# Kernel optimization log

Hardware: AMD Instinct MI355X
Metric: run time of the kernel (lower is better)

The kernel has to match this reference:

```python
import jax, jax.numpy as jnp
import numpy as np

N, E, B = 50000, 800000, 64
F_IN, HID, H, L = 128, 128, 4, 4
C = HID // H  # per-head channels = 32
NEG_SLOPE = 0.2  # PyG GATConv default leaky_relu slope


def setup_inputs() -> dict:
    key = jax.random.key(0)
    ks = iter(jax.random.split(key, 32))
    rn = lambda shape, s=0.05: jax.random.normal(next(ks), shape, jnp.float32) * s
    x = jax.random.normal(next(ks), (N, F_IN), jnp.float32)
    edge_index = jax.random.randint(next(ks), (2, E), 0, N, jnp.int32)
    edge_attr = jax.random.uniform(next(ks), (E, 2), dtype=jnp.float32)
    batch = jnp.sort(jax.random.randint(next(ks), (N,), 0, B, jnp.int32))
    return {
        "x": x, "edge_attr": edge_attr,
        "Win": rn((F_IN, HID)), "b_in": jnp.zeros((HID,), jnp.float32),
        "We1": rn((2, 16)), "be1": jnp.zeros((16,), jnp.float32),
        "We2": rn((16, H)), "be2": jnp.zeros((H,), jnp.float32),
        "Wl": rn((L, HID, HID)), "a_src": rn((L, H, C)), "a_dst": rn((L, H, C)),
        "bl": jnp.zeros((L, HID), jnp.float32),
        "ln_g": jnp.ones((L, HID), jnp.float32), "ln_b": jnp.zeros((L, HID), jnp.float32),
        "Wg1": rn((HID, HID // 2)), "bg1": jnp.zeros((HID // 2,), jnp.float32),
        "Wg2": rn((HID // 2, 1)), "bg2": jnp.zeros((1,), jnp.float32),
        "edge_index": edge_index, "batch": batch,
    }


def _layer_norm(x, g, b, eps=1e-5):
    mu = x.mean(-1, keepdims=True)
    var = ((x - mu) ** 2).mean(-1, keepdims=True)
    return (x - mu) * jax.lax.rsqrt(var + eps) * g + b


def _gat_conv(h, src, dst, W, a_s, a_d, bias):
    # PyG GATConv (shared lin for src/dst), add_self_loops already in src/dst.
    xp = (h @ W).reshape(N, H, C)            # [N,H,C]
    as_n = (xp * a_s).sum(-1)                # [N,H]
    ad_n = (xp * a_d).sum(-1)                # [N,H]
    e = jax.nn.leaky_relu(as_n[src] + ad_n[dst], NEG_SLOPE)   # [E+N,H]
    m = jax.ops.segment_max(e, dst, num_segments=N)           # stable softmax per dst
    p = jnp.exp(e - m[dst])
    s = jax.ops.segment_sum(p, dst, num_segments=N)
    alpha = p / (s[dst] + 1e-16)
    out = jax.ops.segment_sum(xp[src] * alpha[..., None], dst, num_segments=N)
    return out.reshape(N, HID) + bias


def reference(x, edge_attr, Win, b_in, We1, be1, We2, be2, Wl, a_src, a_dst, bl,
              ln_g, ln_b, Wg1, bg1, Wg2, bg2, edge_index, batch):
    h = x @ Win + b_in                                   # input_proj
    # edge bias MLP -> per-edge scalar -> scatter_add crit_signal (no self loops)
    edge_bias = jax.nn.relu(edge_attr @ We1 + be1) @ We2 + be2   # [E,H]
    edge_scalar = edge_bias.mean(axis=1)                         # [E]
    crit = jnp.zeros((N,), h.dtype).at[edge_index[1]].add(edge_scalar)[:, None]
    # self loops for GATConv
    loop = jnp.arange(N, dtype=edge_index.dtype)
    src = jnp.concatenate([edge_index[0], loop])
    dst = jnp.concatenate([edge_index[1], loop])
    for i in range(L):  # fixed small layer count
        h_new = _gat_conv(h, src, dst, Wl[i], a_src[i], a_dst[i], bl[i])
        h_new = _layer_norm(h_new, ln_g[i], ln_b[i])
        h_new = h_new + crit                             # broadcast [N,1]
        h = h_new + h                                    # residual (shapes match); dropout=eval noop
    # GlobalAttention pooling: softmax(gate) over each graph, weighted sum
    gate = jnp.tanh(h @ Wg1 + bg1) @ Wg2 + bg2           # [N,1]
    gmax = jax.ops.segment_max(gate, batch, num_segments=B)
    gp = jnp.exp(gate - gmax[batch])
    gs = jax.ops.segment_sum(gp, batch, num_segments=B)
    gate_sm = gp / (gs[batch] + 1e-16)
    return jax.ops.segment_sum(gate_sm * h, batch, num_segments=B)   # [B,HID]
```

## Files before the change

### kernel.cpp

```cpp
#include <hip/hip_runtime.h>
#include <math.h>

#define N_NODES 50000
#define N_EDGES 800000
#define N_B     64

typedef __attribute__((ext_vector_type(8))) short v8s;
typedef __attribute__((ext_vector_type(4))) float v4f;

__device__ __forceinline__ float lrelu(float x){ return x > 0.f ? x : 0.2f*x; }
__device__ __forceinline__ unsigned short f2b(float f){
  unsigned u = __float_as_uint(f);
  return (unsigned short)((u + 0x7fffu + ((u >> 16) & 1u)) >> 16);
}
__device__ __forceinline__ float blo(unsigned u){ return __uint_as_float(u << 16); }
__device__ __forceinline__ float bhi(unsigned u){ return __uint_as_float(u & 0xffff0000u); }

__global__ void k_conv(const float* __restrict__ Win, const float* __restrict__ Wl,
                       const float* __restrict__ a_src, const float* __restrict__ a_dst,
                       const float* __restrict__ Wg1,
                       unsigned short* __restrict__ WinT, unsigned short* __restrict__ WlT,
                       unsigned short* __restrict__ Wg1T){
  int i = blockIdx.x*256 + threadIdx.x;
  if (i < 16384){
    int n = i >> 7, k = i & 127;
    WinT[n*128+k] = f2b(Win[k*128+n]);
    return;
  }
  i -= 16384;
  if (i < 65536){
    int l = i >> 14, n = (i >> 7) & 127, k = i & 127;
    WlT[l*144*128 + n*128 + k] = f2b(Wl[l*16384 + k*128 + n]);
    return;
  }
  i -= 65536;
  if (i < 4096){
    int l = i >> 10, k = (i >> 3) & 127, t = i & 7;
    int hh = t & 3, sd = t >> 2;
    const float* av = (sd ? a_dst : a_src) + l*128 + hh*32;
    const float* wr = Wl + l*16384 + k*128 + hh*32;
    float s = 0.f;
    #pragma unroll
    for (int c = 0; c < 32; c++) s = fmaf(wr[c], av[c], s);
    WlT[l*144*128 + (128 + sd*4 + hh)*128 + k] = f2b(s);
    return;
  }
  i -= 4096;
  if (i < 4096){
    int l = i >> 10, r = (i >> 7) & 7, k = i & 127;
    WlT[l*144*128 + (136+r)*128 + k] = 0;
    return;
  }
  i -= 4096;
  if (i < 8192){
    int n = i >> 7, k = i & 127;
    Wg1T[n*128+k] = f2b(Wg1[k*64+n]);
  }
}

__global__ void k_setup(const int* __restrict__ batch, int* __restrict__ start,
                        int* __restrict__ cnt){
  int i = blockIdx.x*256 + threadIdx.x;
  if (i >= N_NODES) return;
  cnt[i] = 0;
  int b = batch[i];
  int bp = (i == 0) ? -1 : batch[i-1];
  for (int j = bp+1; j <= b; j++) start[j] = i;
  if (i == N_NODES-1){
    for (int j = b+1; j <= N_B; j++) start[j] = N_NODES;
  }
}

__global__ void k_hist(const int* __restrict__ ei, int* __restrict__ cnt, int* __restrict__ rank){
  int t = blockIdx.x*256 + threadIdx.x;
  if (t >= 200000) return;
  #pragma unroll
  for (int r = 0; r < 4; r++){
    int e = t + r*200000;
    int d = ei[N_EDGES + e];
    rank[e] = atomicAdd(&cnt[d], 1);
  }
}

__global__ void k_scan1(const int* __restrict__ cnt, int* __restrict__ incl, int* __restrict__ part){
  __shared__ int sh[256];
  int tid = threadIdx.x, i = blockIdx.x*256 + tid;
  int v = (i < N_NODES) ? cnt[i] : 0;
  sh[tid] = v; __syncthreads();
  for (int off = 1; off < 256; off <<= 1){
    int t = (tid >= off) ? sh[tid-off] : 0;
    __syncthreads();
    sh[tid] += t; __syncthreads();
  }
  if (i < N_NODES) incl[i] = sh[tid];
  if (tid == 255) part[blockIdx.x] = sh[255];
}
__global__ void k_scan23(const int* __restrict__ cnt, const int* __restrict__ incl,
                         const int* __restrict__ part, int* __restrict__ off){
  __shared__ int red[4];
  __shared__ int bsum;
  int tid = threadIdx.x, lane = tid & 63, wave = tid >> 6;
  int v = (tid < (int)blockIdx.x) ? part[tid] : 0;
  #pragma unroll
  for (int m = 1; m < 64; m <<= 1) v += __shfl_xor(v, m);
  if (lane == 0) red[wave] = v;
  __syncthreads();
  if (tid == 0) bsum = red[0]+red[1]+red[2]+red[3];
  __syncthreads();
  int i = blockIdx.x*256 + tid;
  if (i >= N_NODES) return;
  int e = incl[i] - cnt[i] + bsum;
  off[i] = e;
  if (i == N_NODES-1) off[N_NODES] = e + cnt[i];
}

__global__ void k_fill(const float* __restrict__ ea, const float* __restrict__ We1,
                       const float* __restrict__ be1, const float* __restrict__ We2,
                       const float* __restrict__ be2, const int* __restrict__ ei,
                       const int* __restrict__ off, const int* __restrict__ rank,
                       int2* __restrict__ es){
  __shared__ float w0[16], w1[16], bb[16], w2s[16];
  __shared__ float b2s;
  int tid = threadIdx.x;
  if (tid < 16){
    w0[tid] = We1[tid]; w1[tid] = We1[16+tid]; bb[tid] = be1[tid];
    w2s[tid] = 0.25f*(We2[tid*4]+We2[tid*4+1]+We2[tid*4+2]+We2[tid*4+3]);
  }
  if (tid == 0) b2s = 0.25f*(be2[0]+be2[1]+be2[2]+be2[3]);
  __syncthreads();
  int t = blockIdx.x*256 + tid;
  if (t >= 200000) return;
  #pragma unroll
  for (int r = 0; r < 4; r++){
    int e = t + r*200000;
    float a0 = ea[2*e], a1 = ea[2*e+1];
    float s = b2s;
    #pragma unroll
    for (int j = 0; j < 16; j++){
      float v = fmaf(a0, w0[j], fmaf(a1, w1[j], bb[j]));
      v = v > 0.f ? v : 0.f;
      s = fmaf(v, w2s[j], s);
    }
    int d = ei[N_EDGES + e];
    int p = off[d] + rank[e];
    es[p] = make_int2(ei[e], __float_as_int(s));
  }
}

template<int NT, int MODE, bool AF32>
__global__ __launch_bounds__(256) void k_mgemm(
    const void* __restrict__ A, const unsigned short* __restrict__ Bt,
    const float* __restrict__ bias,
    float* __restrict__ h, unsigned short* __restrict__ hb,
    unsigned short* __restrict__ xpb, float* __restrict__ asn, float* __restrict__ adn,
    const float* __restrict__ Wg2, const float* __restrict__ bg2, float* __restrict__ gate)
{
  __shared__ __attribute__((aligned(16))) unsigned short Bs[NT*16][136];
  __shared__ __attribute__((aligned(16))) unsigned short As[4][16][136];
  int tid = threadIdx.x, wave = tid >> 6, lane = tid & 63;
  int l15 = lane & 15, quad = lane >> 4;
  int rbase = blockIdx.x * 64;
  for (int id = tid; id < NT*16*16; id += 256){
    int r = id >> 4, ch = id & 15;
    *(v8s*)&Bs[r][ch*8] = *(const v8s*)(Bt + r*128 + ch*8);
  }
  for (int id = tid; id < 64*16; id += 256){
    int r = id >> 4, ch = id & 15;
    int gr = rbase + r;
    v8s v = {0,0,0,0,0,0,0,0};
    if (gr < N_NODES){
      if (AF32){
        const float* Af = (const float*)A + (size_t)gr*128 + ch*8;
        float4 va = *(const float4*)Af;
        float4 vb = *(const float4*)(Af + 4);
        v[0]=(short)f2b(va.x); v[1]=(short)f2b(va.y); v[2]=(short)f2b(va.z); v[3]=(short)f2b(va.w);
        v[4]=(short)f2b(vb.x); v[5]=(short)f2b(vb.y); v[6]=(short)f2b(vb.z); v[7]=(short)f2b(vb.w);
      } else {
        v = *(const v8s*)((const unsigned short*)A + (size_t)gr*128 + ch*8);
      }
    }
    *(v8s*)&As[r >> 4][r & 15][ch*8] = v;
  }
  __syncthreads();
  v4f acc[NT];
  #pragma unroll
  for (int t = 0; t < NT; t++) acc[t] = (v4f){0.f,0.f,0.f,0.f};
  #pragma unroll
  for (int kb = 0; kb < 4; kb++){
    v8s a = *(v8s*)&As[wave][l15][kb*32 + quad*8];
    #pragma unroll
    for (int ct = 0; ct < NT; ct++){
      v8s b = *(v8s*)&Bs[ct*16 + l15][kb*32 + quad*8];
      acc[ct] = __builtin_amdgcn_mfma_f32_16x16x32_bf16(a, b, acc[ct], 0, 0, 0);
    }
  }
  int row0 = rbase + wave*16 + quad*4;
  if (MODE == 0){
    #pragma unroll
    for (int ct = 0; ct < 8; ct++){
      float bcol = bias[ct*16 + l15];
      #pragma unroll
      for (int r = 0; r < 4; r++){
        int gr = row0 + r;
        if (gr < N_NODES){
          float v = acc[ct][r] + bcol;
          h[(size_t)gr*128 + ct*16 + l15] = v;
          hb[(size_t)gr*128 + ct*16 + l15] = f2b(v);
        }
      }
    }
  } else if (MODE == 1){
    #pragma unroll
    for (int ct = 0; ct < 8; ct++){
      #pragma unroll
      for (int r = 0; r < 4; r++){
        int gr = row0 + r;
        if (gr < N_NODES) xpb[(size_t)gr*128 + ct*16 + l15] = f2b(acc[ct][r]);
      }
    }
    #pragma unroll
    for (int r = 0; r < 4; r++){
      int gr = row0 + r;
      if (gr < N_NODES){
        float v = acc[NT-1][r];
        if (l15 < 4) asn[gr*4 + l15] = v;
        else if (l15 < 8) adn[gr*4 + (l15-4)] = v;
      }
    }
  } else {
    float part[4] = {0.f,0.f,0.f,0.f};
    #pragma unroll
    for (int ct = 0; ct < NT; ct++){
      float b1 = bias[ct*16 + l15];
      float w2 = Wg2[ct*16 + l15];
      #pragma unroll
      for (int r = 0; r < 4; r++) part[r] = fmaf(tanhf(acc[ct][r] + b1), w2, part[r]);
    }
    #pragma unroll
    for (int m = 1; m < 16; m <<= 1){
      #pragma unroll
      for (int r = 0; r < 4; r++) part[r] += __shfl_xor(part[r], m);
    }
    if (l15 == 0){
      float b2 = bg2[0];
      #pragma unroll
      for (int r = 0; r < 4; r++){
        int gr = row0 + r;
        if (gr < N_NODES) gate[gr] = part[r] + b2;
      }
    }
  }
}

template<bool CRIT>
__global__ __launch_bounds__(256) void k_aggr(
    const unsigned short* __restrict__ xpb, const float* __restrict__ asn,
    const float* __restrict__ adn, const int* __restrict__ off,
    const int2* __restrict__ es,
    const float* __restrict__ bl, const float* __restrict__ lng,
    const float* __restrict__ lnb, float* __restrict__ crit,
    float* __restrict__ h, unsigned short* __restrict__ hb)
{
  __shared__ float lp[4][256];
  int wave = threadIdx.x >> 6, lane = threadIdx.x & 63;
  int n = blockIdx.x*4 + wave;
  if (n >= N_NODES) return;
  int base = off[n], deg = off[n+1] - base;
  float4 ad4 = *(const float4*)(adn + n*4);
  float4 asf = *(const float4*)(asn + n*4);
  float ex = lrelu(asf.x+ad4.x), ey = lrelu(asf.y+ad4.y);
  float ez = lrelu(asf.z+ad4.z), ew = lrelu(asf.w+ad4.w);
  const unsigned* xw = (const unsigned*)xpb;
  float* myp = &lp[wave][0];
  int hh = lane >> 4;
  float acc0, acc1, sx, sy, sz, sw, cr;
  float psx, psy, psz, psw;

  if (deg <= 64){
    int sreg = 0;
    float e0 = -3.0e38f, e1 = -3.0e38f, e2 = -3.0e38f, e3 = -3.0e38f;
    float cw = 0.f;
    if (lane < deg){
      int2 er = es[base + lane];
      sreg = er.x;
      float4 a = *(const float4*)(asn + sreg*4);
      e0 = lrelu(a.x+ad4.x); e1 = lrelu(a.y+ad4.y);
      e2 = lrelu(a.z+ad4.z); e3 = lrelu(a.w+ad4.w);
      if (CRIT) cw = __int_as_float(er.y);
    }
    float mx = fmaxf(e0,ex), my = fmaxf(e1,ey), mz = fmaxf(e2,ez), mw = fmaxf(e3,ew);
    #pragma unroll
    for (int m = 1; m < 64; m <<= 1){
      mx = fmaxf(mx, __shfl_xor(mx, m)); my = fmaxf(my, __shfl_xor(my, m));
      mz = fmaxf(mz, __shfl_xor(mz, m)); mw = fmaxf(mw, __shfl_xor(mw, m));
      if (CRIT) cw += __shfl_xor(cw, m);
    }
    if (CRIT){ if (lane == 0) crit[n] = cw; cr = cw; }
    else cr = crit[n];
    psx = __expf(ex-mx); psy = __expf(ey-my); psz = __expf(ez-mz); psw = __expf(ew-mw);
    float p0 = 0.f, p1 = 0.f, p2 = 0.f, p3 = 0.f;
    if (lane < deg){
      p0 = __expf(e0-mx); p1 = __expf(e1-my); p2 = __expf(e2-mz); p3 = __expf(e3-mw);
    }
    sx = p0; sy = p1; sz = p2; sw = p3;
    *(float4*)(&myp[4*lane]) = make_float4(p0,p1,p2,p3);
    __threadfence_block();
    float pself = hh < 2 ? (hh == 0 ? psx : psy) : (hh == 2 ? psz : psw);
    unsigned us = (xw + ((size_t)(unsigned)n << 6))[lane];
    acc0 = pself * blo(us); acc1 = pself * bhi(us);
    int degR = (deg + 7) & ~7;
    for (int c = 0; c < degR; c += 8){
      unsigned u[8];
      #pragma unroll
      for (int k = 0; k < 8; k++){
        int s0 = __builtin_amdgcn_readlane(sreg, c + k);
        u[k] = (xw + ((size_t)(unsigned)s0 << 6))[lane];
      }
      #pragma unroll
      for (int k = 0; k < 8; k++){
        float q = myp[4*(c+k) + hh];
        acc0 = fmaf(q, blo(u[k]), acc0);
        acc1 = fmaf(q, bhi(u[k]), acc1);
      }
    }
    __threadfence_block();
  } else {
    float mx = ex, my = ey, mz = ez, mw = ew;
    float cw = 0.f;
    for (int j = lane; j < deg; j += 64){
      int2 er = es[base + j];
      float4 a = *(const float4*)(asn + er.x*4);
      mx = fmaxf(mx, lrelu(a.x+ad4.x)); my = fmaxf(my, lrelu(a.y+ad4.y));
      mz = fmaxf(mz, lrelu(a.z+ad4.z)); mw = fmaxf(mw, lrelu(a.w+ad4.w));
      if (CRIT) cw += __int_as_float(er.y);
    }
    #pragma unroll
    for (int m = 1; m < 64; m <<= 1){
      mx = fmaxf(mx, __shfl_xor(mx, m)); my = fmaxf(my, __shfl_xor(my, m));
      mz = fmaxf(mz, __shfl_xor(mz, m)); mw = fmaxf(mw, __shfl_xor(mw, m));
      if (CRIT) cw += __shfl_xor(cw, m);
    }
    if (CRIT){ if (lane == 0) crit[n] = cw; cr = cw; }
    else cr = crit[n];
    psx = __expf(ex-mx); psy = __expf(ey-my); psz = __expf(ez-mz); psw = __expf(ew-mw);
    float pself = hh < 2 ? (hh == 0 ? psx : psy) : (hh == 2 ? psz : psw);
    unsigned us = (xw + ((size_t)(unsigned)n << 6))[lane];
    acc0 = pself * blo(us); acc1 = pself * bhi(us);
    sx = 0.f; sy = 0.f; sz = 0.f; sw = 0.f;
    for (int j0 = 0; j0 < deg; j0 += 64){
      int clen = deg - j0; if (clen > 64) clen = 64;
      int sreg = 0;
      float p0 = 0.f, p1 = 0.f, p2 = 0.f, p3 = 0.f;
      if (lane < clen){
        sreg = es[base + j0 + lane].x;
        float4 a = *(const float4*)(asn + sreg*4);
        p0 = __expf(lrelu(a.x+ad4.x)-mx);
        p1 = __expf(lrelu(a.y+ad4.y)-my);
        p2 = __expf(lrelu(a.z+ad4.z)-mz);
        p3 = __expf(lrelu(a.w+ad4.w)-mw);
        sx += p0; sy += p1; sz += p2; sw += p3;
      }
      *(float4*)(&myp[4*lane]) = make_float4(p0,p1,p2,p3);
      __threadfence_block();
      int clenR = (clen + 7) & ~7;
      for (int c = 0; c < clenR; c += 8){
        unsigned u[8];
        #pragma unroll
        for (int k = 0; k < 8; k++){
          int s0 = __builtin_amdgcn_readlane(sreg, c + k);
          u[k] = (xw + ((size_t)(unsigned)s0 << 6))[lane];
        }
        #pragma unroll
        for (int k = 0; k < 8; k++){
          float q = myp[4*(c+k) + hh];
          acc0 = fmaf(q, blo(u[k]), acc0);
          acc1 = fmaf(q, bhi(u[k]), acc1);
        }
      }
      __threadfence_block();
    }
  }
  #pragma unroll
  for (int m = 1; m < 64; m <<= 1){
    sx += __shfl_xor(sx, m); sy += __shfl_xor(sy, m);
    sz += __shfl_xor(sz, m); sw += __shfl_xor(sw, m);
  }
  sx += psx; sy += psy; sz += psz; sw += psw;
  float den = (hh < 2 ? (hh == 0 ? sx : sy) : (hh == 2 ? sz : sw)) + 1e-16f;
  float rden = 1.f / den;
  int c0 = 2*lane;
  float2 blv = *(const float2*)(bl + c0);
  float o0 = acc0*rden + blv.x;
  float o1 = acc1*rden + blv.y;
  float su = o0 + o1, sq = o0*o0 + o1*o1;
  #pragma unroll
  for (int m = 1; m < 64; m <<= 1){ su += __shfl_xor(su, m); sq += __shfl_xor(sq, m); }
  float mu  = su * (1.f/128.f);
  float var = sq * (1.f/128.f) - mu*mu; var = var > 0.f ? var : 0.f;
  float inv = rsqrtf(var + 1e-5f);
  float2 rv  = *(const float2*)(h + (size_t)n*128 + c0);
  float2 gv  = *(const float2*)(lng + c0);
  float2 bv2 = *(const float2*)(lnb + c0);
  o0 = (o0-mu)*inv*gv.x + bv2.x + cr + rv.x;
  o1 = (o1-mu)*inv*gv.y + bv2.y + cr + rv.y;
  *(float2*)(&h[(size_t)n*128 + c0]) = make_float2(o0, o1);
  *(unsigned*)(&hb[(size_t)n*128 + c0]) = ((unsigned)f2b(o1) << 16) | f2b(o0);
}

__global__ __launch_bounds__(256) void k_pool(
    const float* __restrict__ h, float* __restrict__ gate,
    const int* __restrict__ start, float* __restrict__ out)
{
  __shared__ float red[4];
  __shared__ float sbc;
  __shared__ float4 accs[8][32];
  int b = blockIdx.x;
  int s0 = start[b], s1 = start[b+1];
  int tid = threadIdx.x, lane = tid & 63, wave = tid >> 6;
  float m = -3.0e38f;
  for (int i = s0 + tid; i < s1; i += 256) m = fmaxf(m, gate[i]);
  #pragma unroll
  for (int k = 1; k < 64; k <<= 1) m = fmaxf(m, __shfl_xor(m, k));
  if (lane == 0) red[wave] = m;
  __syncthreads();
  if (tid == 0) sbc = fmaxf(fmaxf(red[0],red[1]), fmaxf(red[2],red[3]));
  __syncthreads();
  float gm = sbc;
  __syncthreads();
  float s = 0.f;
  for (int i = s0 + tid; i < s1; i += 256){
    float p = __expf(gate[i] - gm);
    gate[i] = p;
    s += p;
  }
  #pragma unroll
  for (int k = 1; k < 64; k <<= 1) s += __shfl_xor(s, k);
  if (lane == 0) red[wave] = s;
  __syncthreads();
  if (tid == 0) sbc = red[0]+red[1]+red[2]+red[3];
  __syncthreads();
  float inv = 1.f / (sbc + 1e-16f);
  int c4 = (tid & 31) * 4;
  int g  = tid >> 5;
  float4 acc = make_float4(0.f,0.f,0.f,0.f);
  for (int i = s0 + g; i < s1; i += 8){
    float p = gate[i];
    float4 hv = *(const float4*)(h + (size_t)i*128 + c4);
    acc.x = fmaf(p,hv.x,acc.x); acc.y = fmaf(p,hv.y,acc.y);
    acc.z = fmaf(p,hv.z,acc.z); acc.w = fmaf(p,hv.w,acc.w);
  }
  accs[g][tid & 31] = acc;
  __syncthreads();
  if (g == 0){
    float4 t = acc;
    #pragma unroll
    for (int k = 1; k < 8; k++){
      float4 o = accs[k][tid & 31];
      t.x += o.x; t.y += o.y; t.z += o.z; t.w += o.w;
    }
    t.x *= inv; t.y *= inv; t.z *= inv; t.w *= inv;
    *(float4*)(out + b*128 + c4) = t;
  }
}

extern "C" void kernel_launch(void* const* d_in, const int* in_sizes, int n_in,
                              void* d_out, int out_size, void* d_ws, size_t ws_size,
                              hipStream_t stream){
  (void)in_sizes; (void)n_in; (void)out_size; (void)ws_size;
  const float* x    = (const float*)d_in[0];
  const float* ea   = (const float*)d_in[1];
  const float* Win  = (const float*)d_in[2];
  const float* b_in = (const float*)d_in[3];
  const float* We1  = (const float*)d_in[4];
  const float* be1  = (const float*)d_in[5];
  const float* We2  = (const float*)d_in[6];
  const float* be2  = (const float*)d_in[7];
  const float* Wl   = (const float*)d_in[8];
  const float* a_src= (const float*)d_in[9];
  const float* a_dst= (const float*)d_in[10];
  const float* bl   = (const float*)d_in[11];
  const float* lng  = (const float*)d_in[12];
  const float* lnb  = (const float*)d_in[13];
  const float* Wg1  = (const float*)d_in[14];
  const float* bg1  = (const float*)d_in[15];
  const float* Wg2  = (const float*)d_in[16];
  const float* bg2  = (const float*)d_in[17];
  const int*   ei   = (const int*)d_in[18];
  const int*   batch= (const int*)d_in[19];
  float* out = (float*)d_out;

  char* w = (char*)d_ws;
  auto alloc = [&](size_t bytes){ char* p = w; w += (bytes + 255) & ~(size_t)255; return p; };
  float* h    = (float*)alloc((size_t)N_NODES*128*4);
  unsigned short* hb  = (unsigned short*)alloc((size_t)N_NODES*128*2);
  unsigned short* xpb = (unsigned short*)alloc((size_t)N_NODES*128*2);
  float* asn  = (float*)alloc((size_t)N_NODES*4*4);
  float* adn  = (float*)alloc((size_t)N_NODES*4*4);
  float* crit = (float*)alloc((size_t)N_NODES*4);
  int*   cnt  = (int*)alloc((size_t)N_NODES*4);
  int*   incl = (int*)alloc((size_t)N_NODES*4);
  int*   part = (int*)alloc(256*4);
  int*   off  = (int*)alloc((size_t)(N_NODES+1)*4);
  int*   rank = (int*)alloc((size_t)N_EDGES*4);
  int2*  es   = (int2*)alloc((size_t)N_EDGES*8);
  float* gate = (float*)alloc((size_t)N_NODES*4);
  int*   start= (int*)alloc((size_t)(N_B+1)*4);
  unsigned short* WinT = (unsigned short*)alloc((size_t)128*128*2);
  unsigned short* WlT  = (unsigned short*)alloc((size_t)4*144*128*2);
  unsigned short* Wg1T = (unsigned short*)alloc((size_t)64*128*2);

  int nb_n = (N_NODES + 255)/256;
  int nb_w = (N_NODES + 3)/4;
  int nb_g = (N_NODES + 63)/64;
  int nb_c = (98304 + 255)/256;
  int nb_4e = (200000 + 255)/256;

  k_conv<<<nb_c,256,0,stream>>>(Win, Wl, a_src, a_dst, Wg1, WinT, WlT, Wg1T);
  k_setup<<<nb_n,256,0,stream>>>(batch, start, cnt);
  k_hist<<<nb_4e,256,0,stream>>>(ei, cnt, rank);
  k_mgemm<8,0,true><<<nb_g,256,0,stream>>>((const void*)x, WinT, b_in, h, hb,
                                           nullptr, nullptr, nullptr, nullptr, nullptr, nullptr);
  k_scan1<<<nb_n,256,0,stream>>>(cnt, incl, part);
  k_scan23<<<nb_n,256,0,stream>>>(cnt, incl, part, off);
  k_fill<<<nb_4e,256,0,stream>>>(ea, We1, be1, We2, be2, ei, off, rank, es);
  for (int l = 0; l < 4; l++){
    k_mgemm<9,1,false><<<nb_g,256,0,stream>>>((const void*)hb, WlT + (size_t)l*144*128, nullptr,
                                              nullptr, nullptr, xpb, asn, adn,
                                              nullptr, nullptr, nullptr);
    if (l == 0)
      k_aggr<true><<<nb_w,256,0,stream>>>(xpb, asn, adn, off, es,
                                          bl + l*128, lng + l*128, lnb + l*128, crit, h, hb);
    else
      k_aggr<false><<<nb_w,256,0,stream>>>(xpb, asn, adn, off, es,
                                           bl + l*128, lng + l*128, lnb + l*128, crit, h, hb);
  }
  k_mgemm<4,2,false><<<nb_g,256,0,stream>>>((const void*)hb, Wg1T, bg1, nullptr, nullptr,
                                            nullptr, nullptr, nullptr, Wg2, bg2, gate);
  k_pool<<<N_B,256,0,stream>>>(h, gate, start, out);
}
```

Measured before the change: 475.8 us.

## Shift GAT softmax by self-loop logit, drop bf16 h copy, merge setup kernels

The attention softmax is now stabilised with each node's self-loop logit instead of a per-destination max. This removes the max-reduction pass and the cross-lane sum shuffles, since each lane accumulates the denominator locally and the self term contributes exactly 1. The separate bf16 copy of h is dropped: GEMMs now read fp32 h and convert while staging into LDS. The weight conversion and batch-setup kernels are merged into one launch, and the aggregation accumulates with packed float2 math. The risk is overflow in exp when a neighbour logit far exceeds the self logit. The GEMMs also read twice as many A bytes.

```diff
diff --git a/kernel.cpp b/kernel.cpp
--- a/kernel.cpp
+++ b/kernel.cpp
@@ -7,6 +7,7 @@
 
 typedef __attribute__((ext_vector_type(8))) short v8s;
 typedef __attribute__((ext_vector_type(4))) float v4f;
+typedef __attribute__((ext_vector_type(2))) float v2f;
 
 __device__ __forceinline__ float lrelu(float x){ return x > 0.f ? x : 0.2f*x; }
 __device__ __forceinline__ unsigned short f2b(float f){
@@ -16,11 +17,24 @@
 __device__ __forceinline__ float blo(unsigned u){ return __uint_as_float(u << 16); }
 __device__ __forceinline__ float bhi(unsigned u){ return __uint_as_float(u & 0xffff0000u); }
 
-__global__ void k_conv(const float* __restrict__ Win, const float* __restrict__ Wl,
-                       const float* __restrict__ a_src, const float* __restrict__ a_dst,
-                       const float* __restrict__ Wg1,
-                       unsigned short* __restrict__ WinT, unsigned short* __restrict__ WlT,
-                       unsigned short* __restrict__ Wg1T){
+__global__ void k_convsetup(const float* __restrict__ Win, const float* __restrict__ Wl,
+                            const float* __restrict__ a_src, const float* __restrict__ a_dst,
+                            const float* __restrict__ Wg1, const int* __restrict__ batch,
+                            unsigned short* __restrict__ WinT, unsigned short* __restrict__ WlT,
+                            unsigned short* __restrict__ Wg1T, int* __restrict__ start,
+                            int* __restrict__ cnt){
+  if (blockIdx.x >= 384){
+    int i = (blockIdx.x - 384)*256 + threadIdx.x;
+    if (i >= N_NODES) return;
+    cnt[i] = 0;
+    int b = batch[i];
+    int bp = (i == 0) ? -1 : batch[i-1];
+    for (int j = bp+1; j <= b; j++) start[j] = i;
+    if (i == N_NODES-1){
+      for (int j = b+1; j <= N_B; j++) start[j] = N_NODES;
+    }
+    return;
+  }
   int i = blockIdx.x*256 + threadIdx.x;
   if (i < 16384){
     int n = i >> 7, k = i & 127;
@@ -55,19 +69,6 @@
   if (i < 8192){
     int n = i >> 7, k = i & 127;
     Wg1T[n*128+k] = f2b(Wg1[k*64+n]);
-  }
-}
-
-__global__ void k_setup(const int* __restrict__ batch, int* __restrict__ start,
-                        int* __restrict__ cnt){
-  int i = blockIdx.x*256 + threadIdx.x;
-  if (i >= N_NODES) return;
-  cnt[i] = 0;
-  int b = batch[i];
-  int bp = (i == 0) ? -1 : batch[i-1];
-  for (int j = bp+1; j <= b; j++) start[j] = i;
-  if (i == N_NODES-1){
-    for (int j = b+1; j <= N_B; j++) start[j] = N_NODES;
   }
 }
 
@@ -147,11 +148,11 @@
   }
 }
 
-template<int NT, int MODE, bool AF32>
+template<int NT, int MODE>
 __global__ __launch_bounds__(256) void k_mgemm(
-    const void* __restrict__ A, const unsigned short* __restrict__ Bt,
+    const float* __restrict__ A, const unsigned short* __restrict__ Bt,
     const float* __restrict__ bias,
-    float* __restrict__ h, unsigned short* __restrict__ hb,
+    float* __restrict__ h,
     unsigned short* __restrict__ xpb, float* __restrict__ asn, float* __restrict__ adn,
     const float* __restrict__ Wg2, const float* __restrict__ bg2, float* __restrict__ gate)
 {
@@ -169,15 +170,11 @@
     int gr = rbase + r;
     v8s v = {0,0,0,0,0,0,0,0};
     if (gr < N_NODES){
-      if (AF32){
-        const float* Af = (const float*)A + (size_t)gr*128 + ch*8;
-        float4 va = *(const float4*)Af;
-        float4 vb = *(const float4*)(Af + 4);
-        v[0]=(short)f2b(va.x); v[1]=(short)f2b(va.y); v[2]=(short)f2b(va.z); v[3]=(short)f2b(va.w);
-        v[4]=(short)f2b(vb.x); v[5]=(short)f2b(vb.y); v[6]=(short)f2b(vb.z); v[7]=(short)f2b(vb.w);
-      } else {
-        v = *(const v8s*)((const unsigned short*)A + (size_t)gr*128 + ch*8);
-      }
+      const float* Af = A + (size_t)gr*128 + ch*8;
+      float4 va = *(const float4*)Af;
+      float4 vb = *(const float4*)(Af + 4);
+      v[0]=(short)f2b(va.x); v[1]=(short)f2b(va.y); v[2]=(short)f2b(va.z); v[3]=(short)f2b(va.w);
+      v[4]=(short)f2b(vb.x); v[5]=(short)f2b(vb.y); v[6]=(short)f2b(vb.z); v[7]=(short)f2b(vb.w);
     }
     *(v8s*)&As[r >> 4][r & 15][ch*8] = v;
   }
@@ -202,11 +199,7 @@
       #pragma unroll
       for (int r = 0; r < 4; r++){
         int gr = row0 + r;
-        if (gr < N_NODES){
-          float v = acc[ct][r] + bcol;
-          h[(size_t)gr*128 + ct*16 + l15] = v;
-          hb[(size_t)gr*128 + ct*16 + l15] = f2b(v);
-        }
+        if (gr < N_NODES) h[(size_t)gr*128 + ct*16 + l15] = acc[ct][r] + bcol;
       }
     }
   } else if (MODE == 1){
@@ -259,7 +252,7 @@
     const int2* __restrict__ es,
     const float* __restrict__ bl, const float* __restrict__ lng,
     const float* __restrict__ lnb, float* __restrict__ crit,
-    float* __restrict__ h, unsigned short* __restrict__ hb)
+    float* __restrict__ h)
 {
   __shared__ float lp[4][256];
   int wave = threadIdx.x >> 6, lane = threadIdx.x & 63;
@@ -273,41 +266,33 @@
   const unsigned* xw = (const unsigned*)xpb;
   float* myp = &lp[wave][0];
   int hh = lane >> 4;
-  float acc0, acc1, sx, sy, sz, sw, cr;
-  float psx, psy, psz, psw;
+  float cr, dsum = 0.f;
+  v2f acc;
+  unsigned us = (xw + ((size_t)(unsigned)n << 6))[lane];
+  acc.x = blo(us); acc.y = bhi(us);
 
   if (deg <= 64){
     int sreg = 0;
-    float e0 = -3.0e38f, e1 = -3.0e38f, e2 = -3.0e38f, e3 = -3.0e38f;
     float cw = 0.f;
+    float p0 = 0.f, p1 = 0.f, p2 = 0.f, p3 = 0.f;
     if (lane < deg){
       int2 er = es[base + lane];
       sreg = er.x;
       float4 a = *(const float4*)(asn + sreg*4);
-      e0 = lrelu(a.x+ad4.x); e1 = lrelu(a.y+ad4.y);
-      e2 = lrelu(a.z+ad4.z); e3 = lrelu(a.w+ad4.w);
+      p0 = __expf(lrelu(a.x+ad4.x) - ex);
+      p1 = __expf(lrelu(a.y+ad4.y) - ey);
+      p2 = __expf(lrelu(a.z+ad4.z) - ez);
+      p3 = __expf(lrelu(a.w+ad4.w) - ew);
       if (CRIT) cw = __int_as_float(er.y);
     }
-    float mx = fmaxf(e0,ex), my = fmaxf(e1,ey), mz = fmaxf(e2,ez), mw = fmaxf(e3,ew);
-    #pragma unroll
-    for (int m = 1; m < 64; m <<= 1){
-      mx = fmaxf(mx, __shfl_xor(mx, m)); my = fmaxf(my, __shfl_xor(my, m));
-      mz = fmaxf(mz, __shfl_xor(mz, m)); mw = fmaxf(mw, __shfl_xor(mw, m));
-      if (CRIT) cw += __shfl_xor(cw, m);
-    }
-    if (CRIT){ if (lane == 0) crit[n] = cw; cr = cw; }
-    else cr = crit[n];
-    psx = __expf(ex-mx); psy = __expf(ey-my); psz = __expf(ez-mz); psw = __expf(ew-mw);
-    float p0 = 0.f, p1 = 0.f, p2 = 0.f, p3 = 0.f;
-    if (lane < deg){
-      p0 = __expf(e0-mx); p1 = __expf(e1-my); p2 = __expf(e2-mz); p3 = __expf(e3-mw);
-    }
-    sx = p0; sy = p1; sz = p2; sw = p3;
+    if (CRIT){
+      #pragma unroll
+      for (int m = 1; m < 64; m <<= 1) cw += __shfl_xor(cw, m);
+      if (lane == 0) crit[n] = cw;
+      cr = cw;
+    } else cr = crit[n];
     *(float4*)(&myp[4*lane]) = make_float4(p0,p1,p2,p3);
     __threadfence_block();
-    float pself = hh < 2 ? (hh == 0 ? psx : psy) : (hh == 2 ? psz : psw);
-    unsigned us = (xw + ((size_t)(unsigned)n << 6))[lane];
-    acc0 = pself * blo(us); acc1 = pself * bhi(us);
     int degR = (deg + 7) & ~7;
     for (int c = 0; c < degR; c += 8){
       unsigned u[8];
@@ -319,34 +304,21 @@
       #pragma unroll
       for (int k = 0; k < 8; k++){
         float q = myp[4*(c+k) + hh];
-        acc0 = fmaf(q, blo(u[k]), acc0);
-        acc1 = fmaf(q, bhi(u[k]), acc1);
+        dsum += q;
+        v2f v = {blo(u[k]), bhi(u[k])};
+        acc += q * v;
       }
     }
     __threadfence_block();
   } else {
-    float mx = ex, my = ey, mz = ez, mw = ew;
-    float cw = 0.f;
-    for (int j = lane; j < deg; j += 64){
-      int2 er = es[base + j];
-      float4 a = *(const float4*)(asn + er.x*4);
-      mx = fmaxf(mx, lrelu(a.x+ad4.x)); my = fmaxf(my, lrelu(a.y+ad4.y));
-      mz = fmaxf(mz, lrelu(a.z+ad4.z)); mw = fmaxf(mw, lrelu(a.w+ad4.w));
-      if (CRIT) cw += __int_as_float(er.y);
-    }
-    #pragma unroll
-    for (int m = 1; m < 64; m <<= 1){
-      mx = fmaxf(mx, __shfl_xor(mx, m)); my = fmaxf(my, __shfl_xor(my, m));
-      mz = fmaxf(mz, __shfl_xor(mz, m)); mw = fmaxf(mw, __shfl_xor(mw, m));
-      if (CRIT) cw += __shfl_xor(cw, m);
-    }
-    if (CRIT){ if (lane == 0) crit[n] = cw; cr = cw; }
-    else cr = crit[n];
-    psx = __expf(ex-mx); psy = __expf(ey-my); psz = __expf(ez-mz); psw = __expf(ew-mw);
-    float pself = hh < 2 ? (hh == 0 ? psx : psy) : (hh == 2 ? psz : psw);
-    unsigned us = (xw + ((size_t)(unsigned)n << 6))[lane];
-    acc0 = pself * blo(us); acc1 = pself * bhi(us);
-    sx = 0.f; sy = 0.f; sz = 0.f; sw = 0.f;
+    if (CRIT){
+      float cw = 0.f;
+      for (int j = lane; j < deg; j += 64) cw += __int_as_float(es[base + j].y);
+      #pragma unroll
+      for (int m = 1; m < 64; m <<= 1) cw += __shfl_xor(cw, m);
+      if (lane == 0) crit[n] = cw;
+      cr = cw;
+    } else cr = crit[n];
     for (int j0 = 0; j0 < deg; j0 += 64){
       int clen = deg - j0; if (clen > 64) clen = 64;
       int sreg = 0;
@@ -354,11 +326,10 @@
       if (lane < clen){
         sreg = es[base + j0 + lane].x;
         float4 a = *(const float4*)(asn + sreg*4);
-        p0 = __expf(lrelu(a.x+ad4.x)-mx);
-        p1 = __expf(lrelu(a.y+ad4.y)-my);
-        p2 = __expf(lrelu(a.z+ad4.z)-mz);
-        p3 = __expf(lrelu(a.w+ad4.w)-mw);
-        sx += p0; sy += p1; sz += p2; sw += p3;
+        p0 = __expf(lrelu(a.x+ad4.x) - ex);
+        p1 = __expf(lrelu(a.y+ad4.y) - ey);
+        p2 = __expf(lrelu(a.z+ad4.z) - ez);
+        p3 = __expf(lrelu(a.w+ad4.w) - ew);
       }
       *(float4*)(&myp[4*lane]) = make_float4(p0,p1,p2,p3);
       __threadfence_block();
@@ -373,25 +344,19 @@
         #pragma unroll
         for (int k = 0; k < 8; k++){
           float q = myp[4*(c+k) + hh];
-          acc0 = fmaf(q, blo(u[k]), acc0);
-          acc1 = fmaf(q, bhi(u[k]), acc1);
+          dsum += q;
+          v2f v = {blo(u[k]), bhi(u[k])};
+          acc += q * v;
         }
       }
       __threadfence_block();
     }
   }
-  #pragma unroll
-  for (int m = 1; m < 64; m <<= 1){
-    sx += __shfl_xor(sx, m); sy += __shfl_xor(sy, m);
-    sz += __shfl_xor(sz, m); sw += __shfl_xor(sw, m);
-  }
-  sx += psx; sy += psy; sz += psz; sw += psw;
-  float den = (hh < 2 ? (hh == 0 ? sx : sy) : (hh == 2 ? sz : sw)) + 1e-16f;
-  float rden = 1.f / den;
+  float rden = 1.f / (dsum + 1.f + 1e-16f);
   int c0 = 2*lane;
   float2 blv = *(const float2*)(bl + c0);
-  float o0 = acc0*rden + blv.x;
-  float o1 = acc1*rden + blv.y;
+  float o0 = acc.x*rden + blv.x;
+  float o1 = acc.y*rden + blv.y;
   float su = o0 + o1, sq = o0*o0 + o1*o1;
   #pragma unroll
   for (int m = 1; m < 64; m <<= 1){ su += __shfl_xor(su, m); sq += __shfl_xor(sq, m); }
@@ -404,7 +369,6 @@
   o0 = (o0-mu)*inv*gv.x + bv2.x + cr + rv.x;
   o1 = (o1-mu)*inv*gv.y + bv2.y + cr + rv.y;
   *(float2*)(&h[(size_t)n*128 + c0]) = make_float2(o0, o1);
-  *(unsigned*)(&hb[(size_t)n*128 + c0]) = ((unsigned)f2b(o1) << 16) | f2b(o0);
 }
 
 __global__ __launch_bounds__(256) void k_pool(
@@ -492,7 +456,6 @@
   char* w = (char*)d_ws;
   auto alloc = [&](size_t bytes){ char* p = w; w += (bytes + 255) & ~(size_t)255; return p; };
   float* h    = (float*)alloc((size_t)N_NODES*128*4);
-  unsigned short* hb  = (unsigned short*)alloc((size_t)N_NODES*128*2);
   unsigned short* xpb = (unsigned short*)alloc((size_t)N_NODES*128*2);
   float* asn  = (float*)alloc((size_t)N_NODES*4*4);
   float* adn  = (float*)alloc((size_t)N_NODES*4*4);
@@ -512,29 +475,28 @@
   int nb_n = (N_NODES + 255)/256;
   int nb_w = (N_NODES + 3)/4;
   int nb_g = (N_NODES + 63)/64;
-  int nb_c = (98304 + 255)/256;
+  int nb_cs = 384 + nb_n;
   int nb_4e = (200000 + 255)/256;
 
-  k_conv<<<nb_c,256,0,stream>>>(Win, Wl, a_src, a_dst, Wg1, WinT, WlT, Wg1T);
-  k_setup<<<nb_n,256,0,stream>>>(batch, start, cnt);
+  k_convsetup<<<nb_cs,256,0,stream>>>(Win, Wl, a_src, a_dst, Wg1, batch,
+                                      WinT, WlT, Wg1T, start, cnt);
   k_hist<<<nb_4e,256,0,stream>>>(ei, cnt, rank);
-  k_mgemm<8,0,true><<<nb_g,256,0,stream>>>((const void*)x, WinT, b_in, h, hb,
-                                           nullptr, nullptr, nullptr, nullptr, nullptr, nullptr);
+  k_mgemm<8,0><<<nb_g,256,0,stream>>>(x, WinT, b_in, h,
+                                      nullptr, nullptr, nullptr, nullptr, nullptr, nullptr);
   k_scan1<<<nb_n,256,0,stream>>>(cnt, incl, part);
   k_scan23<<<nb_n,256,0,stream>>>(cnt, incl, part, off);
   k_fill<<<nb_4e,256,0,stream>>>(ea, We1, be1, We2, be2, ei, off, rank, es);
   for (int l = 0; l < 4; l++){
-    k_mgemm<9,1,false><<<nb_g,256,0,stream>>>((const void*)hb, WlT + (size_t)l*144*128, nullptr,
-                                              nullptr, nullptr, xpb, asn, adn,
-                                              nullptr, nullptr, nullptr);
+    k_mgemm<9,1><<<nb_g,256,0,stream>>>(h, WlT + (size_t)l*144*128, nullptr, nullptr,
+                                        xpb, asn, adn, nullptr, nullptr, nullptr);
     if (l == 0)
       k_aggr<true><<<nb_w,256,0,stream>>>(xpb, asn, adn, off, es,
-                                          bl + l*128, lng + l*128, lnb + l*128, crit, h, hb);
+                                          bl + l*128, lng + l*128, lnb + l*128, crit, h);
     else
       k_aggr<false><<<nb_w,256,0,stream>>>(xpb, asn, adn, off, es,
-                                           bl + l*128, lng + l*128, lnb + l*128, crit, h, hb);
-  }
-  k_mgemm<4,2,false><<<nb_g,256,0,stream>>>((const void*)hb, Wg1T, bg1, nullptr, nullptr,
-                                            nullptr, nullptr, nullptr, Wg2, bg2, gate);
+                                           bl + l*128, lng + l*128, lnb + l*128, crit, h);
+  }
+  k_mgemm<4,2><<<nb_g,256,0,stream>>>(h, Wg1T, bg1, nullptr,
+                                      nullptr, nullptr, nullptr, Wg2, bg2, gate);
   k_pool<<<N_B,256,0,stream>>>(h, gate, start, out);
 }
```

New measurement: 440.1 us. 1.08x faster.
